# Performance work log

Measured on AMD Instinct MI355X. Metric: run time of the kernel, lower is better.

The kernel has to match this reference:

```python
import jax, jax.numpy as jnp
import numpy as np

N_NODES = 50000
N_EDGES = 600000
D_IN = 128
D_HID = 1024
D_OUT = 128


def setup_inputs() -> dict:
    key = jax.random.key(0)
    ks = jax.random.split(key, 8)
    feat = jax.random.normal(ks[0], (N_NODES, D_IN), dtype=jnp.float32)
    edge_feat = jax.random.normal(ks[1], (N_EDGES, D_IN), dtype=jnp.float32)
    src = jax.random.randint(ks[2], (N_EDGES,), 0, N_NODES, dtype=jnp.int32)
    dst = jax.random.randint(ks[3], (N_EDGES,), 0, N_NODES, dtype=jnp.int32)
    W1 = jax.random.normal(ks[4], (D_IN, D_HID), dtype=jnp.float32) * (1.0 / np.sqrt(D_IN))
    b1 = jnp.zeros((D_HID,), dtype=jnp.float32)
    W2 = jax.random.normal(ks[5], (D_HID, D_OUT), dtype=jnp.float32) * (1.0 / np.sqrt(D_HID))
    b2 = jnp.zeros((D_OUT,), dtype=jnp.float32)
    return {"feat": feat, "edge_feat": edge_feat, "src": src, "dst": dst,
            "W1": W1, "b1": b1, "W2": W2, "b2": b2}


def reference(feat, edge_feat, src, dst, W1, b1, W2, b2):
    # DGL u_add_e: message m_e = h_src(e) + e_feat(e)   [E, D_IN]
    messages = feat[src] + edge_feat
    # reduce sum over incoming edges at each destination node -> [N, D_IN]
    h = jax.ops.segment_sum(messages, dst, num_segments=N_NODES)
    # 2-layer MLP
    h = jax.nn.relu(h @ W1 + b1)
    return h @ W2 + b2
```

## Files before the change

kernel.cpp:

```cpp
#include <hip/hip_runtime.h>
#include <hip/hip_bf16.h>

#define N_NODES 50000
#define N_EDGES 600000
#define D_IN    128
#define D_HID   1024
#define D_OUT   128

#define WS_H      0
#define WS_EID    12800000
#define WS_OFF    15200000
#define WS_CURSOR 15400016
#define WS_DEG    15600016
#define WS_BSUM   15800016
#define WS_W1T    15801040
#define WS_W2T    16063184

typedef short bf16x8 __attribute__((ext_vector_type(8)));
typedef float f32x4  __attribute__((ext_vector_type(4)));

__global__ __launch_bounds__(256) void hist_kernel(
    const int* __restrict__ dst, int* __restrict__ deg)
{
    int e = blockIdx.x * blockDim.x + threadIdx.x;
    if (e < N_EDGES) atomicAdd(&deg[dst[e]], 1);
}

__global__ __launch_bounds__(256) void scan1_kernel(
    const int* __restrict__ deg, int* __restrict__ bsum)
{
    __shared__ int red[256];
    int t = threadIdx.x;
    int idx = blockIdx.x * 256 + t;
    red[t] = (idx < N_NODES) ? deg[idx] : 0;
    __syncthreads();
    for (int s = 128; s > 0; s >>= 1) {
        if (t < s) red[t] += red[t + s];
        __syncthreads();
    }
    if (t == 0) bsum[blockIdx.x] = red[0];
}

#define SCAN_NB 196
__global__ __launch_bounds__(256) void scan2_kernel(
    int* __restrict__ bsum, int* __restrict__ off)
{
    __shared__ int sh[256];
    int t = threadIdx.x;
    int v = (t < SCAN_NB) ? bsum[t] : 0;
    sh[t] = v;
    __syncthreads();
    for (int ofs = 1; ofs < 256; ofs <<= 1) {
        int u = (t >= ofs) ? sh[t - ofs] : 0;
        __syncthreads();
        sh[t] += u;
        __syncthreads();
    }
    if (t < SCAN_NB) bsum[t] = sh[t] - v;
    if (t == 255) off[N_NODES] = sh[255];
}

__global__ __launch_bounds__(256) void scan3_kernel(
    const int* __restrict__ deg, const int* __restrict__ bsum,
    int* __restrict__ off, int* __restrict__ cursor)
{
    __shared__ int sh[256];
    int t = threadIdx.x;
    int idx = blockIdx.x * 256 + t;
    int v = (idx < N_NODES) ? deg[idx] : 0;
    sh[t] = v;
    __syncthreads();
    for (int ofs = 1; ofs < 256; ofs <<= 1) {
        int u = (t >= ofs) ? sh[t - ofs] : 0;
        __syncthreads();
        sh[t] += u;
        __syncthreads();
    }
    if (idx < N_NODES) {
        int ex = bsum[blockIdx.x] + sh[t] - v;
        off[idx] = ex;
        cursor[idx] = ex;
    }
}

__global__ __launch_bounds__(256) void fill_kernel(
    const int* __restrict__ dst, int* __restrict__ cursor, int* __restrict__ eid)
{
    int e = blockIdx.x * blockDim.x + threadIdx.x;
    if (e < N_EDGES) {
        int pos = atomicAdd(&cursor[dst[e]], 1);
        eid[pos] = e;
    }
}

__global__ __launch_bounds__(256) void transpose_cvt_kernel(
    const float* __restrict__ in, __hip_bfloat16* __restrict__ outp,
    int rows, int cols)
{
    __shared__ float tile[32][33];
    int c0 = blockIdx.x * 32, r0 = blockIdx.y * 32;
    int tx = threadIdx.x & 31, ty = threadIdx.x >> 5;
    #pragma unroll
    for (int i = 0; i < 32; i += 8) {
        int r = r0 + ty + i, c = c0 + tx;
        tile[ty + i][tx] = (r < rows && c < cols) ? in[(size_t)r * cols + c] : 0.f;
    }
    __syncthreads();
    #pragma unroll
    for (int i = 0; i < 32; i += 8) {
        int c = c0 + ty + i, r = r0 + tx;
        if (r < rows && c < cols)
            outp[(size_t)c * rows + r] = __float2bfloat16(tile[tx][ty + i]);
    }
}

__global__ __launch_bounds__(256) void gather_kernel(
    const float* __restrict__ feat,
    const float* __restrict__ edge_feat,
    const int*   __restrict__ src,
    const int*   __restrict__ eid,
    const int*   __restrict__ off,
    __hip_bfloat16* __restrict__ hbf)
{
    const int wv   = __builtin_amdgcn_readfirstlane(threadIdx.x >> 6);
    const int lane = threadIdx.x & 63;
    const int n = blockIdx.x * 4 + wv;
    if (n >= N_NODES) return;

    int i   = __builtin_amdgcn_readfirstlane(off[n]);
    int end = __builtin_amdgcn_readfirstlane(off[n + 1]);

    float2 a0 = make_float2(0.f, 0.f), a1 = a0, a2 = a0, a3 = a0;

    for (; i + 3 < end; i += 4) {
        int e0 = __builtin_amdgcn_readfirstlane(eid[i]);
        int e1 = __builtin_amdgcn_readfirstlane(eid[i + 1]);
        int e2 = __builtin_amdgcn_readfirstlane(eid[i + 2]);
        int e3 = __builtin_amdgcn_readfirstlane(eid[i + 3]);
        int s0 = __builtin_amdgcn_readfirstlane(src[e0]);
        int s1 = __builtin_amdgcn_readfirstlane(src[e1]);
        int s2 = __builtin_amdgcn_readfirstlane(src[e2]);
        int s3 = __builtin_amdgcn_readfirstlane(src[e3]);
        float2 f0 = ((const float2*)(edge_feat + (size_t)e0 * D_IN))[lane];
        float2 g0 = ((const float2*)(feat      + (size_t)s0 * D_IN))[lane];
        float2 f1 = ((const float2*)(edge_feat + (size_t)e1 * D_IN))[lane];
        float2 g1 = ((const float2*)(feat      + (size_t)s1 * D_IN))[lane];
        float2 f2 = ((const float2*)(edge_feat + (size_t)e2 * D_IN))[lane];
        float2 g2 = ((const float2*)(feat      + (size_t)s2 * D_IN))[lane];
        float2 f3 = ((const float2*)(edge_feat + (size_t)e3 * D_IN))[lane];
        float2 g3 = ((const float2*)(feat      + (size_t)s3 * D_IN))[lane];
        a0.x += f0.x + g0.x;  a0.y += f0.y + g0.y;
        a1.x += f1.x + g1.x;  a1.y += f1.y + g1.y;
        a2.x += f2.x + g2.x;  a2.y += f2.y + g2.y;
        a3.x += f3.x + g3.x;  a3.y += f3.y + g3.y;
    }
    for (; i < end; ++i) {
        int e = __builtin_amdgcn_readfirstlane(eid[i]);
        int s = __builtin_amdgcn_readfirstlane(src[e]);
        float2 f = ((const float2*)(edge_feat + (size_t)e * D_IN))[lane];
        float2 g = ((const float2*)(feat      + (size_t)s * D_IN))[lane];
        a0.x += f.x + g.x;  a0.y += f.y + g.y;
    }
    float sx = (a0.x + a1.x) + (a2.x + a3.x);
    float sy = (a0.y + a1.y) + (a2.y + a3.y);
    __hip_bfloat162 hv;
    hv.x = __float2bfloat16(sx);
    hv.y = __float2bfloat16(sy);
    ((__hip_bfloat162*)(hbf + (size_t)n * D_IN))[lane] = hv;
}

#define HS_STRIDE 136
#define QS_STRIDE 72

__global__ __launch_bounds__(256) void mlp_mfma_kernel(
    const __hip_bfloat16* __restrict__ hbf,
    const __hip_bfloat16* __restrict__ w1t,
    const float* __restrict__ b1,
    const __hip_bfloat16* __restrict__ w2t,
    const float* __restrict__ b2,
    float* __restrict__ out)
{
    __shared__ __align__(16) short h_s[64 * HS_STRIDE];
    __shared__ __align__(16) short q_s[64 * QS_STRIDE];

    const int t    = threadIdx.x;
    const int wv   = t >> 6;
    const int lane = t & 63;
    const int half = lane >> 4;
    const int lid  = lane & 15;
    const int nb   = blockIdx.x * 64;

    const short* hs  = (const short*)hbf;
    const short* w1s = (const short*)w1t;
    const short* w2s = (const short*)w2t;

    for (int u = t; u < 64 * 16; u += 256) {
        int r = u >> 4, c = u & 15;
        int row = nb + r;
        uint4 v = make_uint4(0u, 0u, 0u, 0u);
        if (row < N_NODES) v = ((const uint4*)(hs + (size_t)row * 128))[c];
        *(uint4*)&h_s[r * HS_STRIDE + c * 8] = v;
    }
    __syncthreads();

    bf16x8 afrag[4][4];
    #pragma unroll
    for (int mt = 0; mt < 4; ++mt)
        #pragma unroll
        for (int ks = 0; ks < 4; ++ks)
            afrag[mt][ks] = *(const bf16x8*)&h_s[(mt * 16 + lid) * HS_STRIDE + ks * 32 + half * 8];

    f32x4 acc[4][2];
    #pragma unroll
    for (int mt = 0; mt < 4; ++mt) {
        acc[mt][0] = f32x4{0.f, 0.f, 0.f, 0.f};
        acc[mt][1] = f32x4{0.f, 0.f, 0.f, 0.f};
    }

    const int ncol1 = wv * 16 + lid;

    for (int jb = 0; jb < D_HID; jb += 64) {
        float bias = b1[jb + ncol1];
        bf16x8 bfrag[4];
        #pragma unroll
        for (int ks = 0; ks < 4; ++ks)
            bfrag[ks] = *(const bf16x8*)&w1s[(size_t)(jb + ncol1) * 128 + ks * 32 + half * 8];

        f32x4 c1[4];
        #pragma unroll
        for (int mt = 0; mt < 4; ++mt) {
            f32x4 c = f32x4{bias, bias, bias, bias};
            #pragma unroll
            for (int ks = 0; ks < 4; ++ks)
                c = __builtin_amdgcn_mfma_f32_16x16x32_bf16(afrag[mt][ks], bfrag[ks], c, 0, 0, 0);
            c1[mt] = c;
        }

        __syncthreads();
        #pragma unroll
        for (int mt = 0; mt < 4; ++mt) {
            #pragma unroll
            for (int r = 0; r < 4; ++r) {
                float v = fmaxf(c1[mt][r], 0.f);
                __hip_bfloat16 bv = __float2bfloat16(v);
                q_s[(mt * 16 + half * 4 + r) * QS_STRIDE + wv * 16 + lid] = *(short*)&bv;
            }
        }
        __syncthreads();

        bf16x8 a2f[4][2];
        #pragma unroll
        for (int mt = 0; mt < 4; ++mt)
            #pragma unroll
            for (int ks = 0; ks < 2; ++ks)
                a2f[mt][ks] = *(const bf16x8*)&q_s[(mt * 16 + lid) * QS_STRIDE + ks * 32 + half * 8];

        #pragma unroll
        for (int nt = 0; nt < 2; ++nt) {
            #pragma unroll
            for (int ks = 0; ks < 2; ++ks) {
                bf16x8 b2f = *(const bf16x8*)&w2s[(size_t)(wv * 32 + nt * 16 + lid) * 1024 + jb + ks * 32 + half * 8];
                #pragma unroll
                for (int mt = 0; mt < 4; ++mt)
                    acc[mt][nt] = __builtin_amdgcn_mfma_f32_16x16x32_bf16(a2f[mt][ks], b2f, acc[mt][nt], 0, 0, 0);
            }
        }
    }

    #pragma unroll
    for (int nt = 0; nt < 2; ++nt) {
        int col = wv * 32 + nt * 16 + lid;
        float bv = b2[col];
        #pragma unroll
        for (int mt = 0; mt < 4; ++mt) {
            #pragma unroll
            for (int r = 0; r < 4; ++r) {
                int row = nb + mt * 16 + half * 4 + r;
                if (row < N_NODES)
                    out[(size_t)row * D_OUT + col] = acc[mt][nt][r] + bv;
            }
        }
    }
}

extern "C" void kernel_launch(void* const* d_in, const int* in_sizes, int n_in,
                              void* d_out, int out_size, void* d_ws, size_t ws_size,
                              hipStream_t stream) {
    const float* feat      = (const float*)d_in[0];
    const float* edge_feat = (const float*)d_in[1];
    const int*   src       = (const int*)d_in[2];
    const int*   dst       = (const int*)d_in[3];
    const float* W1        = (const float*)d_in[4];
    const float* b1        = (const float*)d_in[5];
    const float* W2        = (const float*)d_in[6];
    const float* b2        = (const float*)d_in[7];
    float* out = (float*)d_out;

    char* ws = (char*)d_ws;
    __hip_bfloat16* hbf    = (__hip_bfloat16*)(ws + WS_H);
    int*   eid    = (int*)(ws + WS_EID);
    int*   off    = (int*)(ws + WS_OFF);
    int*   cursor = (int*)(ws + WS_CURSOR);
    int*   deg    = (int*)(ws + WS_DEG);
    int*   bsum   = (int*)(ws + WS_BSUM);
    __hip_bfloat16* w1t = (__hip_bfloat16*)(ws + WS_W1T);
    __hip_bfloat16* w2t = (__hip_bfloat16*)(ws + WS_W2T);

    hipMemsetAsync(deg, 0, (size_t)N_NODES * sizeof(int), stream);

    hist_kernel<<<(N_EDGES + 255) / 256, 256, 0, stream>>>(dst, deg);
    scan1_kernel<<<SCAN_NB, 256, 0, stream>>>(deg, bsum);
    scan2_kernel<<<1, 256, 0, stream>>>(bsum, off);
    scan3_kernel<<<SCAN_NB, 256, 0, stream>>>(deg, bsum, off, cursor);
    fill_kernel<<<(N_EDGES + 255) / 256, 256, 0, stream>>>(dst, cursor, eid);

    transpose_cvt_kernel<<<dim3(1024 / 32, 128 / 32), 256, 0, stream>>>(W1, w1t, D_IN, D_HID);
    transpose_cvt_kernel<<<dim3(128 / 32, 1024 / 32), 256, 0, stream>>>(W2, w2t, D_HID, D_OUT);

    gather_kernel<<<(N_NODES + 3) / 4, 256, 0, stream>>>(feat, edge_feat, src, eid, off, hbf);

    mlp_mfma_kernel<<<(N_NODES + 63) / 64, 256, 0, stream>>>(hbf, w1t, b1, w2t, b2, out);
}
```

Baseline: 612.9 us.

## Fuse gather into MLP kernel and pre-convert node features to bf16

Merges the edge gather/segment-sum into the MFMA MLP kernel, so each block aggregates its 64 nodes straight into shared memory and the bf16 h intermediate no longer round-trips through global memory. Node features are converted to bf16 once up front, halving gather bytes for the random feat reads, and the two weight transposes plus the feat conversion share a single launch. The gather now splits edges across half-waves using float4 loads. The fused kernel has only 782 blocks and runs its gather sequentially per wave, which may lower latency hiding. Rounding feat to bf16 before summation adds some precision loss.

New measurement: 710.0 us. +15.8%, slower.

```diff
diff --git a/kernel.cpp b/kernel.cpp
--- a/kernel.cpp
+++ b/kernel.cpp
@@ -7,7 +7,7 @@
 #define D_HID   1024
 #define D_OUT   128
 
-#define WS_H      0
+#define WS_FEATB  0
 #define WS_EID    12800000
 #define WS_OFF    15200000
 #define WS_CURSOR 15400016
@@ -19,6 +19,14 @@
 typedef short bf16x8 __attribute__((ext_vector_type(8)));
 typedef float f32x4  __attribute__((ext_vector_type(4)));
 
+__device__ __forceinline__ float bf2f(unsigned short u) {
+    union { unsigned int i; float f; } v; v.i = ((unsigned int)u) << 16; return v.f;
+}
+__device__ __forceinline__ unsigned short f2bf(float x) {
+    __hip_bfloat16 b = __float2bfloat16(x);
+    return *(unsigned short*)&b;
+}
+
 __global__ __launch_bounds__(256) void hist_kernel(
     const int* __restrict__ dst, int* __restrict__ deg)
 {
@@ -26,6 +34,7 @@
     if (e < N_EDGES) atomicAdd(&deg[dst[e]], 1);
 }
 
+#define SCAN_NB 196
 __global__ __launch_bounds__(256) void scan1_kernel(
     const int* __restrict__ deg, int* __restrict__ bsum)
 {
@@ -41,7 +50,6 @@
     if (t == 0) bsum[blockIdx.x] = red[0];
 }
 
-#define SCAN_NB 196
 __global__ __launch_bounds__(256) void scan2_kernel(
     int* __restrict__ bsum, int* __restrict__ off)
 {
@@ -93,90 +101,49 @@
     }
 }
 
-__global__ __launch_bounds__(256) void transpose_cvt_kernel(
-    const float* __restrict__ in, __hip_bfloat16* __restrict__ outp,
-    int rows, int cols)
+__global__ __launch_bounds__(256) void cvt_kernel(
+    const float* __restrict__ W1, const float* __restrict__ W2,
+    const float* __restrict__ feat,
+    unsigned short* __restrict__ w1t, unsigned short* __restrict__ w2t,
+    unsigned short* __restrict__ featb)
 {
     __shared__ float tile[32][33];
-    int c0 = blockIdx.x * 32, r0 = blockIdx.y * 32;
-    int tx = threadIdx.x & 31, ty = threadIdx.x >> 5;
-    #pragma unroll
-    for (int i = 0; i < 32; i += 8) {
-        int r = r0 + ty + i, c = c0 + tx;
-        tile[ty + i][tx] = (r < rows && c < cols) ? in[(size_t)r * cols + c] : 0.f;
-    }
-    __syncthreads();
-    #pragma unroll
-    for (int i = 0; i < 32; i += 8) {
-        int c = c0 + ty + i, r = r0 + tx;
-        if (r < rows && c < cols)
-            outp[(size_t)c * rows + r] = __float2bfloat16(tile[tx][ty + i]);
-    }
-}
-
-__global__ __launch_bounds__(256) void gather_kernel(
-    const float* __restrict__ feat,
+    int b = blockIdx.x;
+    if (b < 256) {
+        const float* in;
+        unsigned short* outp;
+        int rows, cols, c0, r0;
+        if (b < 128) { in = W1; outp = w1t; rows = 128;  cols = 1024; c0 = (b & 31) * 32;        r0 = (b >> 5) * 32; }
+        else         { in = W2; outp = w2t; rows = 1024; cols = 128;  c0 = ((b - 128) & 3) * 32; r0 = ((b - 128) >> 2) * 32; }
+        int tx = threadIdx.x & 31, ty = threadIdx.x >> 5;
+        #pragma unroll
+        for (int i = 0; i < 32; i += 8)
+            tile[ty + i][tx] = in[(size_t)(r0 + ty + i) * cols + c0 + tx];
+        __syncthreads();
+        #pragma unroll
+        for (int i = 0; i < 32; i += 8)
+            outp[(size_t)(c0 + ty + i) * rows + r0 + tx] = f2bf(tile[tx][ty + i]);
+    } else {
+        size_t base = (size_t)(b - 256) * 1024 + (size_t)threadIdx.x * 4;
+        float4 v = *(const float4*)(feat + base);
+        ushort4 o;
+        o.x = f2bf(v.x); o.y = f2bf(v.y); o.z = f2bf(v.z); o.w = f2bf(v.w);
+        *(ushort4*)(featb + base) = o;
+    }
+}
+
+#define HS_STRIDE 136
+#define QS_STRIDE 72
+
+__global__ __launch_bounds__(256) void fused_gnn_kernel(
+    const unsigned short* __restrict__ featb,
     const float* __restrict__ edge_feat,
     const int*   __restrict__ src,
     const int*   __restrict__ eid,
     const int*   __restrict__ off,
-    __hip_bfloat16* __restrict__ hbf)
-{
-    const int wv   = __builtin_amdgcn_readfirstlane(threadIdx.x >> 6);
-    const int lane = threadIdx.x & 63;
-    const int n = blockIdx.x * 4 + wv;
-    if (n >= N_NODES) return;
-
-    int i   = __builtin_amdgcn_readfirstlane(off[n]);
-    int end = __builtin_amdgcn_readfirstlane(off[n + 1]);
-
-    float2 a0 = make_float2(0.f, 0.f), a1 = a0, a2 = a0, a3 = a0;
-
-    for (; i + 3 < end; i += 4) {
-        int e0 = __builtin_amdgcn_readfirstlane(eid[i]);
-        int e1 = __builtin_amdgcn_readfirstlane(eid[i + 1]);
-        int e2 = __builtin_amdgcn_readfirstlane(eid[i + 2]);
-        int e3 = __builtin_amdgcn_readfirstlane(eid[i + 3]);
-        int s0 = __builtin_amdgcn_readfirstlane(src[e0]);
-        int s1 = __builtin_amdgcn_readfirstlane(src[e1]);
-        int s2 = __builtin_amdgcn_readfirstlane(src[e2]);
-        int s3 = __builtin_amdgcn_readfirstlane(src[e3]);
-        float2 f0 = ((const float2*)(edge_feat + (size_t)e0 * D_IN))[lane];
-        float2 g0 = ((const float2*)(feat      + (size_t)s0 * D_IN))[lane];
-        float2 f1 = ((const float2*)(edge_feat + (size_t)e1 * D_IN))[lane];
-        float2 g1 = ((const float2*)(feat      + (size_t)s1 * D_IN))[lane];
-        float2 f2 = ((const float2*)(edge_feat + (size_t)e2 * D_IN))[lane];
-        float2 g2 = ((const float2*)(feat      + (size_t)s2 * D_IN))[lane];
-        float2 f3 = ((const float2*)(edge_feat + (size_t)e3 * D_IN))[lane];
-        float2 g3 = ((const float2*)(feat      + (size_t)s3 * D_IN))[lane];
-        a0.x += f0.x + g0.x;  a0.y += f0.y + g0.y;
-        a1.x += f1.x + g1.x;  a1.y += f1.y + g1.y;
-        a2.x += f2.x + g2.x;  a2.y += f2.y + g2.y;
-        a3.x += f3.x + g3.x;  a3.y += f3.y + g3.y;
-    }
-    for (; i < end; ++i) {
-        int e = __builtin_amdgcn_readfirstlane(eid[i]);
-        int s = __builtin_amdgcn_readfirstlane(src[e]);
-        float2 f = ((const float2*)(edge_feat + (size_t)e * D_IN))[lane];
-        float2 g = ((const float2*)(feat      + (size_t)s * D_IN))[lane];
-        a0.x += f.x + g.x;  a0.y += f.y + g.y;
-    }
-    float sx = (a0.x + a1.x) + (a2.x + a3.x);
-    float sy = (a0.y + a1.y) + (a2.y + a3.y);
-    __hip_bfloat162 hv;
-    hv.x = __float2bfloat16(sx);
-    hv.y = __float2bfloat16(sy);
-    ((__hip_bfloat162*)(hbf + (size_t)n * D_IN))[lane] = hv;
-}
-
-#define HS_STRIDE 136
-#define QS_STRIDE 72
-
-__global__ __launch_bounds__(256) void mlp_mfma_kernel(
-    const __hip_bfloat16* __restrict__ hbf,
-    const __hip_bfloat16* __restrict__ w1t,
+    const unsigned short* __restrict__ w1s,
     const float* __restrict__ b1,
-    const __hip_bfloat16* __restrict__ w2t,
+    const unsigned short* __restrict__ w2s,
     const float* __restrict__ b2,
     float* __restrict__ out)
 {
@@ -186,22 +153,60 @@
     const int t    = threadIdx.x;
     const int wv   = t >> 6;
     const int lane = t & 63;
+    const int nb   = blockIdx.x * 64;
+    const int c    = lane & 31;
+    const int p    = lane >> 5;
+
+    for (int j = 0; j < 16; ++j) {
+        const int r = wv * 16 + j;
+        const int n = nb + r;
+        float4 accA = make_float4(0.f, 0.f, 0.f, 0.f);
+        float4 accB = accA;
+        if (n < N_NODES) {
+            int i   = off[n];
+            int end = off[n + 1];
+            for (; i + 3 < end; i += 4) {
+                int e0 = eid[i + p];
+                int e1 = eid[i + 2 + p];
+                int s0 = src[e0];
+                int s1 = src[e1];
+                float4  f0 = ((const float4*)(edge_feat + (size_t)e0 * D_IN))[c];
+                ushort4 g0 = ((const ushort4*)featb)[(size_t)s0 * 32 + c];
+                float4  f1 = ((const float4*)(edge_feat + (size_t)e1 * D_IN))[c];
+                ushort4 g1 = ((const ushort4*)featb)[(size_t)s1 * 32 + c];
+                accA.x += f0.x + bf2f(g0.x); accA.y += f0.y + bf2f(g0.y);
+                accA.z += f0.z + bf2f(g0.z); accA.w += f0.w + bf2f(g0.w);
+                accB.x += f1.x + bf2f(g1.x); accB.y += f1.y + bf2f(g1.y);
+                accB.z += f1.z + bf2f(g1.z); accB.w += f1.w + bf2f(g1.w);
+            }
+            for (; i < end; i += 2) {
+                int idx = i + p;
+                int e = eid[idx < end ? idx : end - 1];
+                int s = src[e];
+                float4  f = ((const float4*)(edge_feat + (size_t)e * D_IN))[c];
+                ushort4 g = ((const ushort4*)featb)[(size_t)s * 32 + c];
+                if (idx < end) {
+                    accA.x += f.x + bf2f(g.x); accA.y += f.y + bf2f(g.y);
+                    accA.z += f.z + bf2f(g.z); accA.w += f.w + bf2f(g.w);
+                }
+            }
+        }
+        float ax = accA.x + accB.x, ay = accA.y + accB.y;
+        float az = accA.z + accB.z, aw = accA.w + accB.w;
+        ax += __shfl_xor(ax, 32);
+        ay += __shfl_xor(ay, 32);
+        az += __shfl_xor(az, 32);
+        aw += __shfl_xor(aw, 32);
+        if (p == 0) {
+            unsigned int lo = (unsigned int)f2bf(ax) | ((unsigned int)f2bf(ay) << 16);
+            unsigned int hi = (unsigned int)f2bf(az) | ((unsigned int)f2bf(aw) << 16);
+            *(uint2*)&h_s[r * HS_STRIDE + c * 4] = make_uint2(lo, hi);
+        }
+    }
+    __syncthreads();
+
     const int half = lane >> 4;
     const int lid  = lane & 15;
-    const int nb   = blockIdx.x * 64;
-
-    const short* hs  = (const short*)hbf;
-    const short* w1s = (const short*)w1t;
-    const short* w2s = (const short*)w2t;
-
-    for (int u = t; u < 64 * 16; u += 256) {
-        int r = u >> 4, c = u & 15;
-        int row = nb + r;
-        uint4 v = make_uint4(0u, 0u, 0u, 0u);
-        if (row < N_NODES) v = ((const uint4*)(hs + (size_t)row * 128))[c];
-        *(uint4*)&h_s[r * HS_STRIDE + c * 8] = v;
-    }
-    __syncthreads();
 
     bf16x8 afrag[4][4];
     #pragma unroll
@@ -229,11 +234,11 @@
         f32x4 c1[4];
         #pragma unroll
         for (int mt = 0; mt < 4; ++mt) {
-            f32x4 c = f32x4{bias, bias, bias, bias};
+            f32x4 cc = f32x4{bias, bias, bias, bias};
             #pragma unroll
             for (int ks = 0; ks < 4; ++ks)
-                c = __builtin_amdgcn_mfma_f32_16x16x32_bf16(afrag[mt][ks], bfrag[ks], c, 0, 0, 0);
-            c1[mt] = c;
+                cc = __builtin_amdgcn_mfma_f32_16x16x32_bf16(afrag[mt][ks], bfrag[ks], cc, 0, 0, 0);
+            c1[mt] = cc;
         }
 
         __syncthreads();
@@ -242,8 +247,7 @@
             #pragma unroll
             for (int r = 0; r < 4; ++r) {
                 float v = fmaxf(c1[mt][r], 0.f);
-                __hip_bfloat16 bv = __float2bfloat16(v);
-                q_s[(mt * 16 + half * 4 + r) * QS_STRIDE + wv * 16 + lid] = *(short*)&bv;
+                q_s[(mt * 16 + half * 4 + r) * QS_STRIDE + wv * 16 + lid] = (short)f2bf(v);
             }
         }
         __syncthreads();
@@ -297,14 +301,14 @@
     float* out = (float*)d_out;
 
     char* ws = (char*)d_ws;
-    __hip_bfloat16* hbf    = (__hip_bfloat16*)(ws + WS_H);
+    unsigned short* featb  = (unsigned short*)(ws + WS_FEATB);
     int*   eid    = (int*)(ws + WS_EID);
     int*   off    = (int*)(ws + WS_OFF);
     int*   cursor = (int*)(ws + WS_CURSOR);
     int*   deg    = (int*)(ws + WS_DEG);
     int*   bsum   = (int*)(ws + WS_BSUM);
-    __hip_bfloat16* w1t = (__hip_bfloat16*)(ws + WS_W1T);
-    __hip_bfloat16* w2t = (__hip_bfloat16*)(ws + WS_W2T);
+    unsigned short* w1t = (unsigned short*)(ws + WS_W1T);
+    unsigned short* w2t = (unsigned short*)(ws + WS_W2T);
 
     hipMemsetAsync(deg, 0, (size_t)N_NODES * sizeof(int), stream);
 
@@ -314,10 +318,9 @@
     scan3_kernel<<<SCAN_NB, 256, 0, stream>>>(deg, bsum, off, cursor);
     fill_kernel<<<(N_EDGES + 255) / 256, 256, 0, stream>>>(dst, cursor, eid);
 
-    transpose_cvt_kernel<<<dim3(1024 / 32, 128 / 32), 256, 0, stream>>>(W1, w1t, D_IN, D_HID);
-    transpose_cvt_kernel<<<dim3(128 / 32, 1024 / 32), 256, 0, stream>>>(W2, w2t, D_HID, D_OUT);
-
-    gather_kernel<<<(N_NODES + 3) / 4, 256, 0, stream>>>(feat, edge_feat, src, eid, off, hbf);
-
-    mlp_mfma_kernel<<<(N_NODES + 63) / 64, 256, 0, stream>>>(hbf, w1t, b1, w2t, b2, out);
-}
+    cvt_kernel<<<256 + (N_NODES * D_IN) / 1024, 256, 0, stream>>>(
+        W1, W2, feat, w1t, w2t, featb);
+
+    fused_gnn_kernel<<<(N_NODES + 63) / 64, 256, 0, stream>>>(
+        featb, edge_feat, src, eid, off, w1t, b1, w2t, b2, out);
+}
```
